# Optimization experiments

Measured on AMD Instinct MI355X. Metric: run time of the kernel, lower is better.

## Reference

```python
import jax, jax.numpy as jnp
import numpy as np

B, L, K, M, N, P, D = 8, 512, 512, 64, 64, 64, 64  # M == D required for residual add


def _layernorm(x, gamma, beta, eps=1e-3):  # keras LayerNormalization default eps
    mu = jnp.mean(x, axis=-1, keepdims=True)
    var = jnp.var(x, axis=-1, keepdims=True)
    return (x - mu) * jax.lax.rsqrt(var + eps) * gamma + beta


def setup_inputs() -> dict:
    key = jax.random.key(0)
    ks = jax.random.split(key, 5)
    return {
        "q": jax.random.normal(ks[0], (B, L, D), dtype=jnp.float32),
        "k": jax.random.normal(ks[1], (B, K, D), dtype=jnp.float32),
        "vq": jax.random.normal(ks[2], (B, L, M, N), dtype=jnp.float32),
        "vk": jax.random.normal(ks[3], (B, K, P, N), dtype=jnp.float32),
        "vexp": jax.random.normal(ks[4], (B, K, P), dtype=jnp.float32),
        "scale": jnp.ones((), dtype=jnp.float32),      # keras Attention use_scale param (init 1)
        "ln_gamma": jnp.ones((D,), dtype=jnp.float32),  # LayerNormalization gamma
        "ln_beta": jnp.zeros((D,), dtype=jnp.float32),  # LayerNormalization beta
    }


def reference(q, k, vq, vk, vexp, scale, ln_gamma, ln_beta):
    # scores: keras Attention with use_scale -> scale * q @ k^T  (B, L, K)
    scores = scale * jnp.einsum('bld,bkd->blk', q, k)
    # no mask in this call path; plain softmax over keys
    weights = jax.nn.softmax(scores, axis=-1)

    # Original value path (materializes 5D 'blkmp'):
    #   s1 = einsum('blmn,bkpn->blkmp', vq, vk)
    #   v  = einsum('blkmp,bkp->blkm', s1, vexp)
    #   out = einsum('blk,blkm->blm', weights, v)
    # Mathematically identical reassociation that never builds the 5D tensor:
    vkc = jnp.einsum('bkpn,bkp->bkn', vk, vexp)       # contract P first
    tmp = jnp.einsum('blk,bkn->bln', weights, vkc)    # softmax-weighted combine over K
    attn_out = jnp.einsum('blmn,bln->blm', vq, tmp)   # contract N -> (B, L, M)

    # BaseAttentionCell / CrossAttention: residual add + LayerNorm
    return _layernorm(q + attn_out, ln_gamma, ln_beta)
```

## Files before the change

kernel.cpp:

```cpp
#include <hip/hip_runtime.h>


__global__ __launch_bounds__(256) void vkc_kernel(const float* __restrict__ vk,
                                                  const float* __restrict__ vexp,
                                                  float* __restrict__ vkc) {
    const int wave = (blockIdx.x << 2) + (threadIdx.x >> 6);
    const int lane = threadIdx.x & 63;

    const float ve_reg = vexp[wave * 64 + lane];
    const int n0 = (lane & 15) << 2;
    const float* base = vk + (long)wave * 4096;

    float ax = 0.f, ay = 0.f, az = 0.f, aw = 0.f;
    #pragma unroll
    for (int it = 0; it < 16; ++it) {
        const int p = (lane >> 4) + (it << 2);
        const float4 v4 = *(const float4*)(base + p * 64 + n0);
        const float w = __shfl(ve_reg, p, 64);
        ax += v4.x * w; ay += v4.y * w; az += v4.z * w; aw += v4.w * w;
    }
    ax += __shfl_down(ax, 32, 64); ax += __shfl_down(ax, 16, 64);
    ay += __shfl_down(ay, 32, 64); ay += __shfl_down(ay, 16, 64);
    az += __shfl_down(az, 32, 64); az += __shfl_down(az, 16, 64);
    aw += __shfl_down(aw, 32, 64); aw += __shfl_down(aw, 16, 64);

    if ((lane & 48) == 0) {
        float4 r; r.x = ax; r.y = ay; r.z = az; r.w = aw;
        *(float4*)(vkc + wave * 64 + n0) = r;
    }
}

__device__ __forceinline__ void lds_barrier() {
    asm volatile("s_waitcnt lgkmcnt(0)" ::: "memory");
    __builtin_amdgcn_s_barrier();
}

__global__ __launch_bounds__(512, 4) void score_out_kernel(
        const float* __restrict__ q,
        const float* __restrict__ k,
        const float* __restrict__ vkc,
        const float* __restrict__ scale_p,
        const float* __restrict__ vq,
        const float* __restrict__ gamma,
        const float* __restrict__ beta,
        float* __restrict__ out) {
    __shared__ float sc[8][512];
    __shared__ float tp[8][8][64];
    __shared__ float tmp_s[8][64];
    __shared__ float attn_s[8][64];

    const int t = threadIdx.x;
    const int wv = t >> 6;
    const int lane = t & 63;
    const int batch = blockIdx.x >> 6;
    const int l0 = (blockIdx.x & 63) << 3;

    const int row = batch * 512 + l0 + wv;
    const float* vql = vq + (long)row * 4096;
    float4 v[16];
    #pragma unroll
    for (int it = 0; it < 16; ++it)
        v[it] = *(const float4*)(vql + it * 256 + lane * 4);
    const float qv = q[row * 64 + lane];

    const float scale = scale_p[0];
    const float* qbase = q + (batch * 512 + l0) * 64;

    {
        const float4* krow = (const float4*)(k + (batch * 512 + t) * 64);
        float acc[8] = {0.f, 0.f, 0.f, 0.f, 0.f, 0.f, 0.f, 0.f};
        #pragma unroll
        for (int dc = 0; dc < 16; ++dc) {
            const float4 kv = krow[dc];
            #pragma unroll
            for (int l = 0; l < 8; ++l) {
                const float4 qv4 = ((const float4*)(qbase + l * 64))[dc];
                acc[l] += qv4.x * kv.x + qv4.y * kv.y + qv4.z * kv.z + qv4.w * kv.w;
            }
        }
        #pragma unroll
        for (int l = 0; l < 8; ++l) sc[l][t] = scale * acc[l];
    }
    lds_barrier();

    {
        float vv[8]; float mx = -1e30f;
        #pragma unroll
        for (int j = 0; j < 8; ++j) { vv[j] = sc[wv][lane + 64 * j]; mx = fmaxf(mx, vv[j]); }
        #pragma unroll
        for (int off = 32; off; off >>= 1) mx = fmaxf(mx, __shfl_xor(mx, off, 64));
        float s = 0.f;
        #pragma unroll
        for (int j = 0; j < 8; ++j) { vv[j] = __expf(vv[j] - mx); s += vv[j]; }
        #pragma unroll
        for (int off = 32; off; off >>= 1) s += __shfl_xor(s, off, 64);
        const float inv = 1.0f / s;
        #pragma unroll
        for (int j = 0; j < 8; ++j) sc[wv][lane + 64 * j] = vv[j] * inv;
    }
    lds_barrier();

    {
        const float* vkcb = vkc + batch * 512 * 64;
        const int ksub = lane >> 4;
        const int n0 = (lane & 15) << 2;
        const int kbeg = wv << 6;
        float4 a[8];
        #pragma unroll
        for (int l = 0; l < 8; ++l) { a[l].x = 0.f; a[l].y = 0.f; a[l].z = 0.f; a[l].w = 0.f; }
        #pragma unroll
        for (int i = 0; i < 16; ++i) {
            const int kk = kbeg + (i << 2) + ksub;
            const float4 v4 = *(const float4*)(vkcb + kk * 64 + n0);
            #pragma unroll
            for (int l = 0; l < 8; ++l) {
                const float w = sc[l][kk];
                a[l].x += w * v4.x; a[l].y += w * v4.y;
                a[l].z += w * v4.z; a[l].w += w * v4.w;
            }
        }
        #pragma unroll
        for (int l = 0; l < 8; ++l) {
            a[l].x += __shfl_down(a[l].x, 32, 64); a[l].x += __shfl_down(a[l].x, 16, 64);
            a[l].y += __shfl_down(a[l].y, 32, 64); a[l].y += __shfl_down(a[l].y, 16, 64);
            a[l].z += __shfl_down(a[l].z, 32, 64); a[l].z += __shfl_down(a[l].z, 16, 64);
            a[l].w += __shfl_down(a[l].w, 32, 64); a[l].w += __shfl_down(a[l].w, 16, 64);
        }
        if (lane < 16) {
            #pragma unroll
            for (int l = 0; l < 8; ++l)
                *(float4*)&tp[wv][l][lane << 2] = a[l];
        }
    }
    lds_barrier();

    {
        float s = tp[0][wv][lane];
        #pragma unroll
        for (int w = 1; w < 8; ++w) s += tp[w][wv][lane];
        tmp_s[wv][lane] = s;
    }

    {
        const int n0 = (lane & 15) << 2;
        const float4 t4 = *(const float4*)&tmp_s[wv][n0];

        #pragma unroll
        for (int it = 0; it < 16; ++it) {
            float part = v[it].x * t4.x + v[it].y * t4.y + v[it].z * t4.z + v[it].w * t4.w;
            part += __shfl_down(part, 8, 16);
            part += __shfl_down(part, 4, 16);
            part += __shfl_down(part, 2, 16);
            part += __shfl_down(part, 1, 16);
            if ((lane & 15) == 0) attn_s[wv][it * 4 + (lane >> 4)] = part;
        }

        const float x = qv + attn_s[wv][lane];
        float s1 = x, s2 = x * x;
        #pragma unroll
        for (int off = 32; off; off >>= 1) {
            s1 += __shfl_xor(s1, off, 64);
            s2 += __shfl_xor(s2, off, 64);
        }
        const float mean = s1 * (1.0f / 64.0f);
        const float var = s2 * (1.0f / 64.0f) - mean * mean;
        const float r = rsqrtf(var + 1e-3f);
        out[row * 64 + lane] = (x - mean) * r * gamma[lane] + beta[lane];
    }
}

extern "C" void kernel_launch(void* const* d_in, const int* in_sizes, int n_in,
                              void* d_out, int out_size, void* d_ws, size_t ws_size,
                              hipStream_t stream) {
    const float* q     = (const float*)d_in[0];
    const float* k     = (const float*)d_in[1];
    const float* vq    = (const float*)d_in[2];
    const float* vk    = (const float*)d_in[3];
    const float* vexp  = (const float*)d_in[4];
    const float* scale = (const float*)d_in[5];
    const float* gamma = (const float*)d_in[6];
    const float* beta  = (const float*)d_in[7];
    float* out = (float*)d_out;

    float* vkc = (float*)d_ws;

    vkc_kernel<<<1024, 256, 0, stream>>>(vk, vexp, vkc);
    score_out_kernel<<<512, 512, 0, stream>>>(q, k, vkc, scale, vq, gamma, beta, out);
}
```

Measured before the change: 193.3 us.

## Fuse vkc reduction into main kernel behind a software grid barrier

```diff
diff --git a/kernel.cpp b/kernel.cpp
--- a/kernel.cpp
+++ b/kernel.cpp
@@ -1,48 +1,80 @@
 #include <hip/hip_runtime.h>
 
 
-__global__ __launch_bounds__(256) void vkc_kernel(const float* __restrict__ vk,
-                                                  const float* __restrict__ vexp,
-                                                  float* __restrict__ vkc) {
-    const int wave = (blockIdx.x << 2) + (threadIdx.x >> 6);
-    const int lane = threadIdx.x & 63;
-
-    const float ve_reg = vexp[wave * 64 + lane];
-    const int n0 = (lane & 15) << 2;
-    const float* base = vk + (long)wave * 4096;
-
-    float ax = 0.f, ay = 0.f, az = 0.f, aw = 0.f;
-    #pragma unroll
-    for (int it = 0; it < 16; ++it) {
-        const int p = (lane >> 4) + (it << 2);
-        const float4 v4 = *(const float4*)(base + p * 64 + n0);
-        const float w = __shfl(ve_reg, p, 64);
-        ax += v4.x * w; ay += v4.y * w; az += v4.z * w; aw += v4.w * w;
-    }
-    ax += __shfl_down(ax, 32, 64); ax += __shfl_down(ax, 16, 64);
-    ay += __shfl_down(ay, 32, 64); ay += __shfl_down(ay, 16, 64);
-    az += __shfl_down(az, 32, 64); az += __shfl_down(az, 16, 64);
-    aw += __shfl_down(aw, 32, 64); aw += __shfl_down(aw, 16, 64);
-
-    if ((lane & 48) == 0) {
-        float4 r; r.x = ax; r.y = ay; r.z = az; r.w = aw;
-        *(float4*)(vkc + wave * 64 + n0) = r;
-    }
-}
+#define NB 512u
 
 __device__ __forceinline__ void lds_barrier() {
     asm volatile("s_waitcnt lgkmcnt(0)" ::: "memory");
     __builtin_amdgcn_s_barrier();
 }
 
-__global__ __launch_bounds__(512, 4) void score_out_kernel(
+__device__ __forceinline__ void grid_barrier(unsigned* cnt, unsigned* gen) {
+    __syncthreads();
+    __threadfence();
+    if (threadIdx.x == 0) {
+        const unsigned g = __hip_atomic_load(gen, __ATOMIC_ACQUIRE,
+                                             __HIP_MEMORY_SCOPE_AGENT);
+        if (__hip_atomic_fetch_add(cnt, 1u, __ATOMIC_ACQ_REL,
+                                   __HIP_MEMORY_SCOPE_AGENT) == NB - 1u) {
+            __hip_atomic_store(cnt, 0u, __ATOMIC_RELAXED,
+                               __HIP_MEMORY_SCOPE_AGENT);
+            __hip_atomic_fetch_add(gen, 1u, __ATOMIC_RELEASE,
+                                   __HIP_MEMORY_SCOPE_AGENT);
+        } else {
+            while (__hip_atomic_load(gen, __ATOMIC_ACQUIRE,
+                                     __HIP_MEMORY_SCOPE_AGENT) == g)
+                __builtin_amdgcn_s_sleep(2);
+        }
+    }
+    __threadfence();
+    __syncthreads();
+}
+
+__global__ __launch_bounds__(256) void kt_kernel(const float* __restrict__ k,
+                                                 float* __restrict__ kT,
+                                                 unsigned* __restrict__ bar) {
+    if (blockIdx.x == 0 && threadIdx.x < 2) bar[threadIdx.x] = 0u;
+
+    __shared__ float tile[64][65];
+    const int b  = blockIdx.x >> 3;
+    const int k0 = (blockIdx.x & 7) << 6;
+    const int t  = threadIdx.x;
+    const int r  = t >> 2;
+    const int c0 = (t & 3) << 4;
+
+    const float* src = k + ((long)(b * 512 + k0 + r)) * 64 + c0;
+    #pragma unroll
+    for (int m = 0; m < 4; ++m) {
+        const float4 v = *(const float4*)(src + 4 * m);
+        tile[r][c0 + 4 * m + 0] = v.x;
+        tile[r][c0 + 4 * m + 1] = v.y;
+        tile[r][c0 + 4 * m + 2] = v.z;
+        tile[r][c0 + 4 * m + 3] = v.w;
+    }
+    __syncthreads();
+    float* dst = kT + ((long)b * 64 + r) * 512 + k0 + c0;
+    #pragma unroll
+    for (int m = 0; m < 4; ++m) {
+        float4 v;
+        v.x = tile[c0 + 4 * m + 0][r];
+        v.y = tile[c0 + 4 * m + 1][r];
+        v.z = tile[c0 + 4 * m + 2][r];
+        v.w = tile[c0 + 4 * m + 3][r];
+        *(float4*)(dst + 4 * m) = v;
+    }
+}
+
+__global__ __launch_bounds__(512, 4) void fused_kernel(
         const float* __restrict__ q,
-        const float* __restrict__ k,
-        const float* __restrict__ vkc,
+        const float* __restrict__ kT,
+        const float* __restrict__ vk,
+        const float* __restrict__ vexp,
         const float* __restrict__ scale_p,
         const float* __restrict__ vq,
         const float* __restrict__ gamma,
         const float* __restrict__ beta,
+        float* __restrict__ vkc,
+        unsigned* __restrict__ bar,
         float* __restrict__ out) {
     __shared__ float sc[8][512];
     __shared__ float tp[8][8][64];
@@ -55,33 +87,60 @@
     const int batch = blockIdx.x >> 6;
     const int l0 = (blockIdx.x & 63) << 3;
 
-    const int row = batch * 512 + l0 + wv;
-    const float* vql = vq + (long)row * 4096;
-    float4 v[16];
-    #pragma unroll
-    for (int it = 0; it < 16; ++it)
-        v[it] = *(const float4*)(vql + it * 256 + lane * 4);
-    const float qv = q[row * 64 + lane];
-
-    const float scale = scale_p[0];
-    const float* qbase = q + (batch * 512 + l0) * 64;
-
-    {
-        const float4* krow = (const float4*)(k + (batch * 512 + t) * 64);
-        float acc[8] = {0.f, 0.f, 0.f, 0.f, 0.f, 0.f, 0.f, 0.f};
+    if (wv >= 4) {
+        const int n0 = (lane & 15) << 2;
+        #pragma unroll
+        for (int rr = 0; rr < 2; ++rr) {
+            const int unit = (blockIdx.x << 3) + ((wv - 4) << 1) + rr;
+            const float ve_reg = vexp[unit * 64 + lane];
+            const float* base = vk + (long)unit * 4096;
+            float ax = 0.f, ay = 0.f, az = 0.f, aw = 0.f;
+            #pragma unroll
+            for (int it = 0; it < 16; ++it) {
+                const int p = (lane >> 4) + (it << 2);
+                const float4 v4 = *(const float4*)(base + p * 64 + n0);
+                const float w = __shfl(ve_reg, p, 64);
+                ax += v4.x * w; ay += v4.y * w; az += v4.z * w; aw += v4.w * w;
+            }
+            ax += __shfl_down(ax, 32, 64); ax += __shfl_down(ax, 16, 64);
+            ay += __shfl_down(ay, 32, 64); ay += __shfl_down(ay, 16, 64);
+            az += __shfl_down(az, 32, 64); az += __shfl_down(az, 16, 64);
+            aw += __shfl_down(aw, 32, 64); aw += __shfl_down(aw, 16, 64);
+            if ((lane & 48) == 0) {
+                float4 r; r.x = ax; r.y = ay; r.z = az; r.w = aw;
+                *(float4*)(vkc + unit * 64 + n0) = r;
+            }
+        }
+    } else {
+        const float scale = scale_p[0];
+        const float* qbase = q + (batch * 512 + l0) * 64;
+        const float* ktb = kT + ((long)batch << 15) + (t << 1);
+        float a0[8], a1[8];
+        #pragma unroll
+        for (int l = 0; l < 8; ++l) { a0[l] = 0.f; a1[l] = 0.f; }
         #pragma unroll
         for (int dc = 0; dc < 16; ++dc) {
-            const float4 kv = krow[dc];
+            float2 kv[4];
+            #pragma unroll
+            for (int j = 0; j < 4; ++j)
+                kv[j] = *(const float2*)(ktb + ((dc << 2) + j) * 512);
             #pragma unroll
             for (int l = 0; l < 8; ++l) {
-                const float4 qv4 = ((const float4*)(qbase + l * 64))[dc];
-                acc[l] += qv4.x * kv.x + qv4.y * kv.y + qv4.z * kv.z + qv4.w * kv.w;
-            }
-        }
-        #pragma unroll
-        for (int l = 0; l < 8; ++l) sc[l][t] = scale * acc[l];
-    }
-    lds_barrier();
+                const float4 qv = ((const float4*)(qbase + l * 64))[dc];
+                a0[l] += qv.x * kv[0].x + qv.y * kv[1].x
+                       + qv.z * kv[2].x + qv.w * kv[3].x;
+                a1[l] += qv.x * kv[0].y + qv.y * kv[1].y
+                       + qv.z * kv[2].y + qv.w * kv[3].y;
+            }
+        }
+        #pragma unroll
+        for (int l = 0; l < 8; ++l) {
+            float2 s2; s2.x = scale * a0[l]; s2.y = scale * a1[l];
+            *(float2*)&sc[l][t << 1] = s2;
+        }
+    }
+
+    grid_barrier(bar, bar + 1);
 
     {
         float vv[8]; float mx = -1e30f;
@@ -142,6 +201,15 @@
     }
 
     {
+        const int row = batch * 512 + l0 + wv;
+        const float* vql = vq + (long)row * 4096;
+
+        float4 v[16];
+        #pragma unroll
+        for (int it = 0; it < 16; ++it)
+            v[it] = *(const float4*)(vql + it * 256 + lane * 4);
+
+        const float qv = q[row * 64 + lane];
         const int n0 = (lane & 15) << 2;
         const float4 t4 = *(const float4*)&tmp_s[wv][n0];
 
@@ -183,7 +251,10 @@
     float* out = (float*)d_out;
 
     float* vkc = (float*)d_ws;
-
-    vkc_kernel<<<1024, 256, 0, stream>>>(vk, vexp, vkc);
-    score_out_kernel<<<512, 512, 0, stream>>>(q, k, vkc, scale, vq, gamma, beta, out);
-}
+    float* kT  = vkc + 8 * 512 * 64;
+    unsigned* bar = (unsigned*)(kT + 8 * 512 * 64);
+
+    kt_kernel<<<64, 256, 0, stream>>>(k, kT, bar);
+    fused_kernel<<<NB, 512, 0, stream>>>(q, kT, vk, vexp, scale, vq,
+                                         gamma, beta, vkc, bar, out);
+}
```

Result: slower. 375.8 us (+94.4%).

## Transpose K in prep kernel for coalesced score loads; defer vq loads

Applied to the files above, without the earlier changes.

```diff
diff --git a/kernel.cpp b/kernel.cpp
--- a/kernel.cpp
+++ b/kernel.cpp
@@ -1,43 +1,77 @@
 #include <hip/hip_runtime.h>
 
-
-__global__ __launch_bounds__(256) void vkc_kernel(const float* __restrict__ vk,
-                                                  const float* __restrict__ vexp,
-                                                  float* __restrict__ vkc) {
-    const int wave = (blockIdx.x << 2) + (threadIdx.x >> 6);
-    const int lane = threadIdx.x & 63;
-
-    const float ve_reg = vexp[wave * 64 + lane];
-    const int n0 = (lane & 15) << 2;
-    const float* base = vk + (long)wave * 4096;
-
-    float ax = 0.f, ay = 0.f, az = 0.f, aw = 0.f;
-    #pragma unroll
-    for (int it = 0; it < 16; ++it) {
-        const int p = (lane >> 4) + (it << 2);
-        const float4 v4 = *(const float4*)(base + p * 64 + n0);
-        const float w = __shfl(ve_reg, p, 64);
-        ax += v4.x * w; ay += v4.y * w; az += v4.z * w; aw += v4.w * w;
-    }
-    ax += __shfl_down(ax, 32, 64); ax += __shfl_down(ax, 16, 64);
-    ay += __shfl_down(ay, 32, 64); ay += __shfl_down(ay, 16, 64);
-    az += __shfl_down(az, 32, 64); az += __shfl_down(az, 16, 64);
-    aw += __shfl_down(aw, 32, 64); aw += __shfl_down(aw, 16, 64);
-
-    if ((lane & 48) == 0) {
-        float4 r; r.x = ax; r.y = ay; r.z = az; r.w = aw;
-        *(float4*)(vkc + wave * 64 + n0) = r;
-    }
-}
 
 __device__ __forceinline__ void lds_barrier() {
     asm volatile("s_waitcnt lgkmcnt(0)" ::: "memory");
     __builtin_amdgcn_s_barrier();
 }
 
-__global__ __launch_bounds__(512, 4) void score_out_kernel(
+__global__ __launch_bounds__(256) void vkc_kt_kernel(const float* __restrict__ vk,
+                                                     const float* __restrict__ vexp,
+                                                     const float* __restrict__ k,
+                                                     float* __restrict__ vkc,
+                                                     float* __restrict__ kT) {
+    __shared__ float tile[64][65];
+
+    {
+        const int wave = (blockIdx.x << 2) + (threadIdx.x >> 6);
+        const int lane = threadIdx.x & 63;
+        const float ve_reg = vexp[wave * 64 + lane];
+        const int n0 = (lane & 15) << 2;
+        const float* base = vk + (long)wave * 4096;
+
+        float ax = 0.f, ay = 0.f, az = 0.f, aw = 0.f;
+        #pragma unroll
+        for (int it = 0; it < 16; ++it) {
+            const int p = (lane >> 4) + (it << 2);
+            const float4 v4 = *(const float4*)(base + p * 64 + n0);
+            const float w = __shfl(ve_reg, p, 64);
+            ax += v4.x * w; ay += v4.y * w; az += v4.z * w; aw += v4.w * w;
+        }
+        ax += __shfl_down(ax, 32, 64); ax += __shfl_down(ax, 16, 64);
+        ay += __shfl_down(ay, 32, 64); ay += __shfl_down(ay, 16, 64);
+        az += __shfl_down(az, 32, 64); az += __shfl_down(az, 16, 64);
+        aw += __shfl_down(aw, 32, 64); aw += __shfl_down(aw, 16, 64);
+
+        if ((lane & 48) == 0) {
+            float4 r; r.x = ax; r.y = ay; r.z = az; r.w = aw;
+            *(float4*)(vkc + wave * 64 + n0) = r;
+        }
+    }
+
+    if (blockIdx.x < 64) {
+        const int b  = blockIdx.x >> 3;
+        const int k0 = (blockIdx.x & 7) << 6;
+        const int t  = threadIdx.x;
+        const int r  = t >> 2;
+        const int c0 = (t & 3) << 4;
+
+        const float* src = k + ((long)(b * 512 + k0 + r)) * 64 + c0;
+        #pragma unroll
+        for (int m = 0; m < 4; ++m) {
+            const float4 v = *(const float4*)(src + 4 * m);
+            tile[r][c0 + 4 * m + 0] = v.x;
+            tile[r][c0 + 4 * m + 1] = v.y;
+            tile[r][c0 + 4 * m + 2] = v.z;
+            tile[r][c0 + 4 * m + 3] = v.w;
+        }
+        __syncthreads();
+        float* dst = kT + ((long)b * 64 + r) * 512 + k0 + c0;
+        #pragma unroll
+        for (int m = 0; m < 4; ++m) {
+            float4 v;
+            v.x = tile[c0 + 4 * m + 0][r];
+            v.y = tile[c0 + 4 * m + 1][r];
+            v.z = tile[c0 + 4 * m + 2][r];
+            v.w = tile[c0 + 4 * m + 3][r];
+            *(float4*)(dst + 4 * m) = v;
+        }
+    }
+}
+
+__global__ __launch_bounds__(512) void score_out_kernel(
         const float* __restrict__ q,
-        const float* __restrict__ k,
+        const float* __restrict__ kT,
         const float* __restrict__ vkc,
         const float* __restrict__ scale_p,
         const float* __restrict__ vq,
@@ -55,27 +89,25 @@
     const int batch = blockIdx.x >> 6;
     const int l0 = (blockIdx.x & 63) << 3;
 
-    const int row = batch * 512 + l0 + wv;
-    const float* vql = vq + (long)row * 4096;
-    float4 v[16];
-    #pragma unroll
-    for (int it = 0; it < 16; ++it)
-        v[it] = *(const float4*)(vql + it * 256 + lane * 4);
-    const float qv = q[row * 64 + lane];
-
     const float scale = scale_p[0];
     const float* qbase = q + (batch * 512 + l0) * 64;
 
     {
-        const float4* krow = (const float4*)(k + (batch * 512 + t) * 64);
-        float acc[8] = {0.f, 0.f, 0.f, 0.f, 0.f, 0.f, 0.f, 0.f};
+        const float* ktb = kT + ((long)batch << 15) + t;
+        float acc[8];
+        #pragma unroll
+        for (int l = 0; l < 8; ++l) acc[l] = 0.f;
         #pragma unroll
         for (int dc = 0; dc < 16; ++dc) {
-            const float4 kv = krow[dc];
+            float kv[4];
+            #pragma unroll
+            for (int j = 0; j < 4; ++j)
+                kv[j] = ktb[((dc << 2) + j) << 9];
             #pragma unroll
             for (int l = 0; l < 8; ++l) {
-                const float4 qv4 = ((const float4*)(qbase + l * 64))[dc];
-                acc[l] += qv4.x * kv.x + qv4.y * kv.y + qv4.z * kv.z + qv4.w * kv.w;
+                const float4 qv = ((const float4*)(qbase + l * 64))[dc];
+                acc[l] += qv.x * kv[0] + qv.y * kv[1]
+                        + qv.z * kv[2] + qv.w * kv[3];
             }
         }
         #pragma unroll
@@ -142,6 +174,15 @@
     }
 
     {
+        const int row = batch * 512 + l0 + wv;
+        const float* vql = vq + (long)row * 4096;
+
+        float4 v[16];
+        #pragma unroll
+        for (int it = 0; it < 16; ++it)
+            v[it] = *(const float4*)(vql + it * 256 + lane * 4);
+
+        const float qv = q[row * 64 + lane];
         const int n0 = (lane & 15) << 2;
         const float4 t4 = *(const float4*)&tmp_s[wv][n0];
 
@@ -183,7 +224,8 @@
     float* out = (float*)d_out;
 
     float* vkc = (float*)d_ws;
-
-    vkc_kernel<<<1024, 256, 0, stream>>>(vk, vexp, vkc);
-    score_out_kernel<<<512, 512, 0, stream>>>(q, k, vkc, scale, vq, gamma, beta, out);
-}
+    float* kT  = vkc + 8 * 512 * 64;
+
+    vkc_kt_kernel<<<1024, 256, 0, stream>>>(vk, vexp, k, vkc, kT);
+    score_out_kernel<<<512, 512, 0, stream>>>(q, kT, vkc, scale, vq, gamma, beta, out);
+}
```

After: 178.6 us. 7.6% less time.
